# Kernel tuning notes

Measured on AMD Instinct MI355X. Metric: run time of the kernel, lower is better.

## Reference

```python
import jax, jax.numpy as jnp
import numpy as np

N_NODES = 100000
N_EDGES = 1600000
NEG_SLOPE = 0.2


def gat_layer(x, edge_index, W, att_src, att_dst, bias, concat):
    """PyG-style GATConv (v1) with self-loops added, dropout=0."""
    N = x.shape[0]
    H, C = att_src.shape
    ar = jnp.arange(N)
    src = jnp.concatenate([edge_index[0], ar])  # add self-loops
    dst = jnp.concatenate([edge_index[1], ar])
    h = (x @ W).reshape(N, H, C)                # [N,H,C]
    a_src = jnp.sum(h * att_src[None], axis=-1)  # [N,H]
    a_dst = jnp.sum(h * att_dst[None], axis=-1)  # [N,H]
    e = jax.nn.leaky_relu(a_src[src] + a_dst[dst], NEG_SLOPE)  # [E,H]
    # segment softmax over destination nodes
    m = jax.ops.segment_max(e, dst, num_segments=N)
    e = jnp.exp(e - m[dst])
    s = jax.ops.segment_sum(e, dst, num_segments=N)
    alpha = e / (s[dst] + 1e-16)                # [E,H]
    msg = h[src] * alpha[:, :, None]            # [E,H,C]
    out = jax.ops.segment_sum(msg, dst, num_segments=N)  # [N,H,C]
    if concat:
        out = out.reshape(N, H * C)
    else:
        out = out.mean(axis=1)
    return out + bias


def prelu(x, a):
    return jnp.where(x >= 0, x, a * x)


def setup_inputs() -> dict:
    key = jax.random.key(0)
    ks = jax.random.split(key, 12)
    def g(k, shape, fan):
        return jax.random.normal(k, shape, dtype=jnp.float32) * (1.0 / np.sqrt(fan))
    x = jax.random.normal(ks[0], (N_NODES, 256), dtype=jnp.float32)
    edge_index = jax.random.randint(ks[1], (2, N_EDGES), 0, N_NODES, dtype=jnp.int64 if jax.config.read('jax_enable_x64') else jnp.int32)
    return {
        'x': x,
        'edge_index': edge_index,
        'W1': g(ks[2], (256, 64), 256), 'as1': g(ks[3], (8, 8), 8), 'ad1': g(ks[4], (8, 8), 8), 'b1': jnp.zeros((64,), jnp.float32),
        'W2': g(ks[5], (320, 64), 320), 'as2': g(ks[6], (8, 8), 8), 'ad2': g(ks[7], (8, 8), 8), 'b2': jnp.zeros((64,), jnp.float32),
        'W3': g(ks[8], (64, 128), 64), 'as3': g(ks[9], (8, 16), 16), 'ad3': g(ks[10], (8, 16), 16), 'b3': jnp.zeros((16,), jnp.float32),
        'p1': jnp.full((1,), 0.25, jnp.float32), 'p2': jnp.full((1,), 0.25, jnp.float32),
    }


def reference(x, edge_index, W1, as1, ad1, b1, W2, as2, ad2, b2, W3, as3, ad3, b3, p1, p2):
    h = gat_layer(x, edge_index, W1, as1, ad1, b1, concat=True)
    h = prelu(h, p1)
    h = gat_layer(jnp.concatenate([x, h], axis=1), edge_index, W2, as2, ad2, b2, concat=True)
    h = prelu(h, p2)
    h = gat_layer(h, edge_index, W3, as3, ad3, b3, concat=False)
    return jax.nn.log_softmax(h, axis=1)
```

## Files before the change

kernel.cpp:

```cpp
#include <hip/hip_runtime.h>
#include <hip/hip_bf16.h>
#include <stdint.h>

typedef unsigned short u16;
typedef __attribute__((ext_vector_type(8))) short short8;
typedef __attribute__((ext_vector_type(8))) __bf16 bf16x8;
typedef __attribute__((ext_vector_type(4))) float f32x4;
typedef __attribute__((ext_vector_type(4))) float fv4;

#define DEV static __device__ __forceinline__

DEV float bf2f(u16 u) { uint32_t i = ((uint32_t)u) << 16; float f; __builtin_memcpy(&f, &i, 4); return f; }
DEV u16 f2bf(float f) {
    uint32_t i; __builtin_memcpy(&i, &f, 4);
    uint32_t r = i + 0x7FFFu + ((i >> 16) & 1u);
    return (u16)(r >> 16);
}
DEV float lo16f(uint32_t u) { uint32_t i = u << 16; float f; __builtin_memcpy(&f, &i, 4); return f; }
DEV float hi16f(uint32_t u) { uint32_t i = u & 0xFFFF0000u; float f; __builtin_memcpy(&f, &i, 4); return f; }
DEV uint32_t pack2(float a, float b) { return (uint32_t)f2bf(a) | ((uint32_t)f2bf(b) << 16); }
DEV float lrelu(float x) { return x >= 0.f ? x : 0.2f * x; }

#define CHK 4096
#define BN2SH 10
#define BN2 1024

__global__ __launch_bounds__(256) void k_cvt(const float* __restrict__ in, u16* __restrict__ out, int n4) {
    int i = blockIdx.x * 256 + threadIdx.x;
    if (i < n4) {
        fv4 v = __builtin_nontemporal_load((const fv4*)in + i);
        ushort4 o;
        o.x = f2bf(v.x); o.y = f2bf(v.y); o.z = f2bf(v.z); o.w = f2bf(v.w);
        ((ushort4*)out)[i] = o;
    }
}

__global__ __launch_bounds__(256) void k_hist(const int* __restrict__ dst, int* __restrict__ hist,
                                              int NBUK, int nbp, int E) {
    __shared__ int h[BN2];
    int tid = threadIdx.x;
    for (int i = tid; i < NBUK; i += 256) h[i] = 0;
    __syncthreads();
    int b0 = blockIdx.x * CHK;
    int jend = b0 + CHK < E ? b0 + CHK : E;
    for (int j = b0 + tid; j < jend; j += 256)
        atomicAdd(&h[dst[j] >> BN2SH], 1);
    __syncthreads();
    for (int i = tid; i < NBUK; i += 256) hist[i * nbp + blockIdx.x] = h[i];
}

__global__ void k_scanpart(const int* __restrict__ deg, int* __restrict__ bsum, int n) {
    __shared__ int buf[1024];
    int tid = threadIdx.x;
    int i = blockIdx.x * 1024 + tid;
    int v = (i < n) ? deg[i] : 0;
    buf[tid] = v; __syncthreads();
    for (int d = 512; d > 0; d >>= 1) {
        if (tid < d) buf[tid] += buf[tid + d];
        __syncthreads();
    }
    if (tid == 0) bsum[blockIdx.x] = buf[0];
}

__global__ void k_scanbsum(int* bsum, int nb) {
    if (threadIdx.x == 0) {
        int run = 0;
        for (int b = 0; b < nb; ++b) { int t = bsum[b]; bsum[b] = run; run += t; }
    }
}

__global__ void k_scanonly(const int* __restrict__ in, const int* __restrict__ bsum,
                           int* __restrict__ out, int n) {
    __shared__ int buf[1024];
    int tid = threadIdx.x;
    int i = blockIdx.x * 1024 + tid;
    int v = (i < n) ? in[i] : 0;
    buf[tid] = v; __syncthreads();
    for (int d = 1; d < 1024; d <<= 1) {
        int t = (tid >= d) ? buf[tid - d] : 0;
        __syncthreads();
        buf[tid] += t;
        __syncthreads();
    }
    if (i < n) out[i] = buf[tid] - v + bsum[blockIdx.x];
}

__global__ __launch_bounds__(256) void k_part(const int* __restrict__ src, const int* __restrict__ dst,
                                              const int* __restrict__ scanned, int2* __restrict__ stage,
                                              int NBUK, int nbp, int E) {
    __shared__ int cur[BN2];
    int tid = threadIdx.x;
    for (int i = tid; i < NBUK; i += 256) cur[i] = scanned[i * nbp + blockIdx.x];
    __syncthreads();
    int b0 = blockIdx.x * CHK;
    int jend = b0 + CHK < E ? b0 + CHK : E;
    for (int j = b0 + tid; j < jend; j += 256) {
        int d = dst[j];
        int p = atomicAdd(&cur[d >> BN2SH], 1);
        stage[p] = make_int2(src[j], d);
    }
}

__global__ __launch_bounds__(256) void k_csr(const int2* __restrict__ stage, const int* __restrict__ scanned,
                                             int* __restrict__ off, int* __restrict__ srt,
                                             int NBUK, int nbp, int N, int E) {
    __shared__ int deg[BN2];
    __shared__ int ex[BN2];
    __shared__ int tsum[256];
    int tid = threadIdx.x, b = blockIdx.x;
    int base = b << BN2SH;
    int s0 = scanned[b * nbp];
    int s1 = (b + 1 < NBUK) ? scanned[(b + 1) * nbp] : E;
    for (int i = tid; i < BN2; i += 256) deg[i] = 0;
    __syncthreads();
    for (int j = s0 + tid; j < s1; j += 256) atomicAdd(&deg[stage[j].y - base], 1);
    __syncthreads();
    int t4 = tid * 4;
    int d0 = deg[t4], d1 = deg[t4 + 1], d2 = deg[t4 + 2], d3 = deg[t4 + 3];
    int tot = d0 + d1 + d2 + d3;
    tsum[tid] = tot; __syncthreads();
    for (int d = 1; d < 256; d <<= 1) {
        int t = (tid >= d) ? tsum[tid - d] : 0;
        __syncthreads();
        tsum[tid] += t;
        __syncthreads();
    }
    int ebase = tsum[tid] - tot;
    ex[t4] = ebase; ex[t4 + 1] = ebase + d0; ex[t4 + 2] = ebase + d0 + d1; ex[t4 + 3] = ebase + d0 + d1 + d2;
    __syncthreads();
    for (int i = tid; i < BN2; i += 256) { int n = base + i; if (n < N) off[n] = s0 + ex[i]; }
    if (b == 0 && tid == 0) off[N] = E;
    __syncthreads();
    for (int j = s0 + tid; j < s1; j += 256) {
        int2 sd = stage[j];
        int p = atomicAdd(&ex[sd.y - base], 1);
        srt[s0 + p] = sd.x;
    }
}

__global__ __launch_bounds__(256) void gemm_k(const u16* __restrict__ A1, int K1,
                                              const u16* __restrict__ A2, int K2,
                                              const float* __restrict__ W, int M,
                                              u16* __restrict__ out, int N) {
    __shared__ u16 wt[64][328];
    __shared__ u16 As[64][40];
    const int K = K1 + K2;
    const int tid = threadIdx.x;
    const int n0 = blockIdx.x * 64;
    const int cb = blockIdx.y * 64;

    for (int idx = tid; idx < K * 64; idx += 256) {
        int k = idx >> 6, m = idx & 63;
        wt[m][k] = f2bf(W[(size_t)k * M + cb + m]);
    }

    const int wv = tid >> 6, lane = tid & 63;
    const int quad = lane >> 4, r = lane & 15;
    f32x4 acc[4];
#pragma unroll
    for (int ct = 0; ct < 4; ++ct) acc[ct] = (f32x4){0.f, 0.f, 0.f, 0.f};

    const int row = tid >> 2, seg = tid & 3;
    const int gl = n0 + row;

    for (int k0 = 0; k0 < K; k0 += 32) {
        int4 v = {0, 0, 0, 0};
        if (gl < N) {
            const u16* base = (k0 < K1) ? (A1 + (size_t)gl * K1 + k0)
                                        : (A2 + (size_t)gl * K2 + (k0 - K1));
            v = *(const int4*)(base + seg * 8);
        }
        *(int4*)&As[row][seg * 8] = v;
        __syncthreads();
        bf16x8 a = __builtin_bit_cast(bf16x8, *(const short8*)&As[wv * 16 + r][quad * 8]);
#pragma unroll
        for (int ct = 0; ct < 4; ++ct) {
            bf16x8 b = __builtin_bit_cast(bf16x8, *(const short8*)&wt[ct * 16 + r][k0 + quad * 8]);
            acc[ct] = __builtin_amdgcn_mfma_f32_16x16x32_bf16(a, b, acc[ct], 0, 0, 0);
        }
        __syncthreads();
    }

#pragma unroll
    for (int ct = 0; ct < 4; ++ct)
#pragma unroll
        for (int rg = 0; rg < 4; ++rg) {
            int grow = n0 + wv * 16 + quad * 4 + rg;
            if (grow < N) out[(size_t)grow * M + cb + ct * 16 + r] = f2bf(acc[ct][rg]);
        }
}

__global__ __launch_bounds__(256) void acomp8(const u16* __restrict__ g,
                                              const float* __restrict__ ats, const float* __restrict__ atd,
                                              float* __restrict__ a_src, float* __restrict__ a_dst, int N) {
    int lane = threadIdx.x & 63;
    int node = blockIdx.x * 4 + (threadIdx.x >> 6);
    if (node >= N) return;
    float val = bf2f(g[(size_t)node * 64 + lane]);
    float ps = val * ats[lane];
    float pd = val * atd[lane];
#pragma unroll
    for (int d = 1; d < 8; d <<= 1) { ps += __shfl_xor(ps, d); pd += __shfl_xor(pd, d); }
    if ((lane & 7) == 0) {
        a_src[node * 8 + (lane >> 3)] = ps;
        a_dst[node * 8 + (lane >> 3)] = pd;
    }
}

__global__ __launch_bounds__(256) void acomp16(const u16* __restrict__ g,
                                               const float* __restrict__ ats, const float* __restrict__ atd,
                                               float* __restrict__ a_src, float* __restrict__ a_dst, int N) {
    int lane = threadIdx.x & 63;
    int node = blockIdx.x * 4 + (threadIdx.x >> 6);
    if (node >= N) return;
    float v0 = bf2f(g[(size_t)node * 128 + lane]);
    float v1 = bf2f(g[(size_t)node * 128 + lane + 64]);
    float ps0 = v0 * ats[lane],      pd0 = v0 * atd[lane];
    float ps1 = v1 * ats[lane + 64], pd1 = v1 * atd[lane + 64];
#pragma unroll
    for (int d = 1; d < 16; d <<= 1) {
        ps0 += __shfl_xor(ps0, d); pd0 += __shfl_xor(pd0, d);
        ps1 += __shfl_xor(ps1, d); pd1 += __shfl_xor(pd1, d);
    }
    if ((lane & 15) == 0) {
        int hd = lane >> 4;
        a_src[node * 8 + hd] = ps0;     a_dst[node * 8 + hd] = pd0;
        a_src[node * 8 + hd + 4] = ps1; a_dst[node * 8 + hd + 4] = pd1;
    }
}

__global__ __launch_bounds__(256) void agg12(const u16* __restrict__ g,
                                             const float* __restrict__ a_src, const float* __restrict__ a_dst,
                                             const int* __restrict__ off, const int* __restrict__ srt,
                                             const float* __restrict__ bias, const float* __restrict__ pslope,
                                             u16* __restrict__ hout, int N) {
    int tid = threadIdx.x;
    int lane32 = tid & 31;
    int node = blockIdx.x * 8 + (tid >> 5);
    int nd = node < N ? node : N - 1;
    int hd = lane32 >> 2;
    int hw = lane32 & 7;
    int e4 = lane32 >> 3;
    float ad_acc = a_dst[nd * 8 + hd];
    float ad_w   = a_dst[nd * 8 + hw];
    float ws = __expf(lrelu(a_src[nd * 8 + hd] + ad_acc));
    uint32_t gs = *(const uint32_t*)(g + (size_t)nd * 64 + lane32 * 2);
    float s = ws;
    float acc0 = ws * lo16f(gs), acc1 = ws * hi16f(gs);
    int jb = off[nd], je = off[nd + 1];
    int addrH = (tid & 32) * 4;
    int addrW = addrH + hd * 4;
    for (int j = jb; j < je; j += 4) {
        int cnt = je - j;
        int jj = j + e4;
        int idx = srt[jj < je ? jj : (je - 1)];
        float w = __expf(lrelu(a_src[idx * 8 + hw] + ad_w));
        int wi = __builtin_bit_cast(int, w);
#pragma unroll
        for (int t = 0; t < 4; ++t) {
            int srcv = __builtin_amdgcn_ds_bpermute(addrH + t * 32, idx);
            int wvi  = __builtin_amdgcn_ds_bpermute(addrW + t * 32, wi);
            float wv = (t < cnt) ? __builtin_bit_cast(float, wvi) : 0.f;
            uint32_t gv = *(const uint32_t*)(g + (size_t)srcv * 64 + lane32 * 2);
            s += wv;
            acc0 += wv * lo16f(gv);
            acc1 += wv * hi16f(gv);
        }
    }
    float r = 1.f / (s + 1e-16f);
    float2 bv = *(const float2*)(bias + lane32 * 2);
    float p = pslope[0];
    float v0 = acc0 * r + bv.x; v0 = v0 >= 0.f ? v0 : p * v0;
    float v1 = acc1 * r + bv.y; v1 = v1 >= 0.f ? v1 : p * v1;
    if (node < N) *(uint32_t*)(hout + (size_t)node * 64 + lane32 * 2) = pack2(v0, v1);
}

__global__ __launch_bounds__(256) void agg3(const u16* __restrict__ g,
                                            const float* __restrict__ a_src, const float* __restrict__ a_dst,
                                            const int* __restrict__ off, const int* __restrict__ srt,
                                            const float* __restrict__ b3, float* __restrict__ out, int N) {
    int tid = threadIdx.x;
    int lane = tid & 63;
    int node = blockIdx.x * 4 + (tid >> 6);
    int nd = node < N ? node : N - 1;
    int hd = lane >> 3;
    int hw = lane & 7;
    float ad_acc = a_dst[nd * 8 + hd];
    float ad_w   = a_dst[nd * 8 + hw];
    float ws = __expf(lrelu(a_src[nd * 8 + hd] + ad_acc));
    uint32_t gs = *(const uint32_t*)(g + (size_t)nd * 128 + lane * 2);
    float s = ws;
    float acc0 = ws * lo16f(gs), acc1 = ws * hi16f(gs);
    int jb = off[nd], je = off[nd + 1];
    int addrW = hd * 4;
    for (int j = jb; j < je; j += 8) {
        int cnt = je - j;
        int jj = j + hd;
        int idx = srt[jj < je ? jj : (je - 1)];
        float w = __expf(lrelu(a_src[idx * 8 + hw] + ad_w));
        int wi = __builtin_bit_cast(int, w);
#pragma unroll
        for (int t = 0; t < 8; ++t) {
            int srcv = __builtin_amdgcn_readlane(idx, t * 8);
            int wvi  = __builtin_amdgcn_ds_bpermute(addrW + t * 32, wi);
            float wv = (t < cnt) ? __builtin_bit_cast(float, wvi) : 0.f;
            uint32_t gv = *(const uint32_t*)(g + (size_t)srcv * 128 + lane * 2);
            s += wv;
            acc0 += wv * lo16f(gv);
            acc1 += wv * hi16f(gv);
        }
    }
    float r = 1.f / (s + 1e-16f);
    float v0 = acc0 * r, v1 = acc1 * r;
    v0 += __shfl_xor(v0, 8);  v1 += __shfl_xor(v1, 8);
    v0 += __shfl_xor(v0, 16); v1 += __shfl_xor(v1, 16);
    v0 += __shfl_xor(v0, 32); v1 += __shfl_xor(v1, 32);
    int c0 = (lane & 7) * 2;
    float2 bv = *(const float2*)(b3 + c0);
    float mean0 = v0 * 0.125f + bv.x, mean1 = v1 * 0.125f + bv.y;
    float m = fmaxf(mean0, mean1);
    m = fmaxf(m, __shfl_xor(m, 1)); m = fmaxf(m, __shfl_xor(m, 2)); m = fmaxf(m, __shfl_xor(m, 4));
    float se = __expf(mean0 - m) + __expf(mean1 - m);
    se += __shfl_xor(se, 1); se += __shfl_xor(se, 2); se += __shfl_xor(se, 4);
    float lg = __logf(se);
    if (node < N && lane < 8) {
        float2 o; o.x = mean0 - m - lg; o.y = mean1 - m - lg;
        *(float2*)(out + (size_t)node * 16 + c0) = o;
    }
}

extern "C" void kernel_launch(void* const* d_in, const int* in_sizes, int n_in,
                              void* d_out, int out_size, void* d_ws, size_t ws_size,
                              hipStream_t stream) {
    (void)n_in; (void)out_size; (void)ws_size;
    const float* x  = (const float*)d_in[0];
    const int* ei   = (const int*)d_in[1];
    const float* W1 = (const float*)d_in[2];
    const float* as1 = (const float*)d_in[3];
    const float* ad1 = (const float*)d_in[4];
    const float* b1  = (const float*)d_in[5];
    const float* W2  = (const float*)d_in[6];
    const float* as2 = (const float*)d_in[7];
    const float* ad2 = (const float*)d_in[8];
    const float* b2  = (const float*)d_in[9];
    const float* W3  = (const float*)d_in[10];
    const float* as3 = (const float*)d_in[11];
    const float* ad3 = (const float*)d_in[12];
    const float* b3  = (const float*)d_in[13];
    const float* p1  = (const float*)d_in[14];
    const float* p2  = (const float*)d_in[15];
    const int N = in_sizes[0] / 256;
    const int E = in_sizes[1] / 2;
    const int NBUK = (N + BN2 - 1) >> BN2SH;
    const int nbp = (E + CHK - 1) / CHK;
    const int nsc = NBUK * nbp;

    char* ws = (char*)d_ws;
    size_t o = 0;
    auto alloc = [&](size_t bytes) { void* p = ws + o; o = (o + bytes + 255) & ~(size_t)255; return p; };
    int* off     = (int*)alloc((size_t)(N + 1) * 4);
    int* bsum    = (int*)alloc(4096);
    int* hist    = (int*)alloc((size_t)nsc * 4);
    int* scanned = (int*)alloc((size_t)nsc * 4);
    int* srt     = (int*)alloc((size_t)E * 4);
    int2* stage  = (int2*)alloc((size_t)E * 8);
    u16* xb      = (u16*)alloc((size_t)N * 256 * 2);
    u16* g       = (u16*)alloc((size_t)N * 128 * 2);
    float* a_src = (float*)alloc((size_t)N * 8 * 4);
    float* a_dst = (float*)alloc((size_t)N * 8 * 4);
    u16* h1      = (u16*)alloc((size_t)N * 64 * 2);
    u16* h2      = (u16*)alloc((size_t)N * 64 * 2);

    int n4 = N * 256 / 4;
    k_cvt<<<(n4 + 255) / 256, 256, 0, stream>>>(x, xb, n4);

    k_hist<<<nbp, 256, 0, stream>>>(ei + E, hist, NBUK, nbp, E);
    int nS = (nsc + 1023) / 1024;
    k_scanpart<<<nS, 1024, 0, stream>>>(hist, bsum, nsc);
    k_scanbsum<<<1, 64, 0, stream>>>(bsum, nS);
    k_scanonly<<<nS, 1024, 0, stream>>>(hist, bsum, scanned, nsc);
    k_part<<<nbp, 256, 0, stream>>>(ei, ei + E, scanned, stage, NBUK, nbp, E);
    k_csr<<<NBUK, 256, 0, stream>>>(stage, scanned, off, srt, NBUK, nbp, N, E);

    int nb64 = (N + 63) / 64;
    int nb4 = (N + 3) / 4;
    int nb8 = (N + 7) / 8;

    gemm_k<<<dim3(nb64, 1), 256, 0, stream>>>(xb, 256, (const u16*)nullptr, 0, W1, 64, g, N);
    acomp8<<<nb4, 256, 0, stream>>>(g, as1, ad1, a_src, a_dst, N);
    agg12<<<nb8, 256, 0, stream>>>(g, a_src, a_dst, off, srt, b1, p1, h1, N);

    gemm_k<<<dim3(nb64, 1), 256, 0, stream>>>(xb, 256, h1, 64, W2, 64, g, N);
    acomp8<<<nb4, 256, 0, stream>>>(g, as2, ad2, a_src, a_dst, N);
    agg12<<<nb8, 256, 0, stream>>>(g, a_src, a_dst, off, srt, b2, p2, h2, N);

    gemm_k<<<dim3(nb64, 2), 256, 0, stream>>>(h2, 64, (const u16*)nullptr, 0, W3, 128, g, N);
    acomp16<<<nb4, 256, 0, stream>>>(g, as3, ad3, a_src, a_dst, N);
    agg3<<<nb4, 256, 0, stream>>>(g, a_src, a_dst, off, srt, b3, (float*)d_out, N);
}
```

Measured before the change: 572.6 us.

## Restructure GAT aggregation to split edges across lanes with 16-byte gathers

The agg12 and agg3 kernels are rewritten so that each wavefront spreads a node's incoming edges across lane slots. Each lane gathers a full 16-byte chunk of a source row (8 bf16 channels) instead of 4 bytes. The per-slot partial sums are then combined with xor-shuffle reductions, which replaces the bpermute/readlane broadcast of indices and weights. This aims to issue fewer, wider memory requests and keep more edges in flight, at the cost of more registers and a reduction tail. The fp32-to-bf16 conversion kernel also switches to a single packed nontemporal 64-bit store.

```diff
diff --git a/kernel.cpp b/kernel.cpp
--- a/kernel.cpp
+++ b/kernel.cpp
@@ -29,9 +29,9 @@
     int i = blockIdx.x * 256 + threadIdx.x;
     if (i < n4) {
         fv4 v = __builtin_nontemporal_load((const fv4*)in + i);
-        ushort4 o;
-        o.x = f2bf(v.x); o.y = f2bf(v.y); o.z = f2bf(v.z); o.w = f2bf(v.w);
-        ((ushort4*)out)[i] = o;
+        uint64_t o = (uint64_t)f2bf(v.x) | ((uint64_t)f2bf(v.y) << 16)
+                   | ((uint64_t)f2bf(v.z) << 32) | ((uint64_t)f2bf(v.w) << 48);
+        __builtin_nontemporal_store(o, (uint64_t*)out + i);
     }
 }
 
@@ -229,50 +229,86 @@
     }
 }
 
+#define ACC8(gv, wgt) do { float _w = (wgt); \
+    s += _w; \
+    acc0 += _w * lo16f((gv).x); acc1 += _w * hi16f((gv).x); \
+    acc2 += _w * lo16f((gv).y); acc3 += _w * hi16f((gv).y); \
+    acc4 += _w * lo16f((gv).z); acc5 += _w * hi16f((gv).z); \
+    acc6 += _w * lo16f((gv).w); acc7 += _w * hi16f((gv).w); \
+} while (0)
+
+#define RED8(d) do { \
+    s    += __shfl_xor(s,    d); \
+    acc0 += __shfl_xor(acc0, d); acc1 += __shfl_xor(acc1, d); \
+    acc2 += __shfl_xor(acc2, d); acc3 += __shfl_xor(acc3, d); \
+    acc4 += __shfl_xor(acc4, d); acc5 += __shfl_xor(acc5, d); \
+    acc6 += __shfl_xor(acc6, d); acc7 += __shfl_xor(acc7, d); \
+} while (0)
+
+#define REDA(d) do { \
+    acc0 += __shfl_xor(acc0, d); acc1 += __shfl_xor(acc1, d); \
+    acc2 += __shfl_xor(acc2, d); acc3 += __shfl_xor(acc3, d); \
+    acc4 += __shfl_xor(acc4, d); acc5 += __shfl_xor(acc5, d); \
+    acc6 += __shfl_xor(acc6, d); acc7 += __shfl_xor(acc7, d); \
+} while (0)
+
 __global__ __launch_bounds__(256) void agg12(const u16* __restrict__ g,
                                              const float* __restrict__ a_src, const float* __restrict__ a_dst,
                                              const int* __restrict__ off, const int* __restrict__ srt,
                                              const float* __restrict__ bias, const float* __restrict__ pslope,
                                              u16* __restrict__ hout, int N) {
     int tid = threadIdx.x;
-    int lane32 = tid & 31;
-    int node = blockIdx.x * 8 + (tid >> 5);
+    int lane = tid & 63;
+    int node = blockIdx.x * 4 + (tid >> 6);
     int nd = node < N ? node : N - 1;
-    int hd = lane32 >> 2;
-    int hw = lane32 & 7;
-    int e4 = lane32 >> 3;
-    float ad_acc = a_dst[nd * 8 + hd];
-    float ad_w   = a_dst[nd * 8 + hw];
-    float ws = __expf(lrelu(a_src[nd * 8 + hd] + ad_acc));
-    uint32_t gs = *(const uint32_t*)(g + (size_t)nd * 64 + lane32 * 2);
-    float s = ws;
-    float acc0 = ws * lo16f(gs), acc1 = ws * hi16f(gs);
+    int cls = lane & 7;
+    int slot = lane >> 3;
+    float ad = a_dst[nd * 8 + cls];
+    float ws = __expf(lrelu(a_src[nd * 8 + cls] + ad));
+    float m0 = (slot == 0) ? ws : 0.f;
+    uint4 gs = *(const uint4*)((const char*)g + ((size_t)nd << 7) + (cls << 4));
+    float s = m0;
+    float acc0 = m0 * lo16f(gs.x), acc1 = m0 * hi16f(gs.x);
+    float acc2 = m0 * lo16f(gs.y), acc3 = m0 * hi16f(gs.y);
+    float acc4 = m0 * lo16f(gs.z), acc5 = m0 * hi16f(gs.z);
+    float acc6 = m0 * lo16f(gs.w), acc7 = m0 * hi16f(gs.w);
     int jb = off[nd], je = off[nd + 1];
-    int addrH = (tid & 32) * 4;
-    int addrW = addrH + hd * 4;
-    for (int j = jb; j < je; j += 4) {
+    for (int j = jb; j < je; j += 16) {
         int cnt = je - j;
-        int jj = j + e4;
-        int idx = srt[jj < je ? jj : (je - 1)];
-        float w = __expf(lrelu(a_src[idx * 8 + hw] + ad_w));
-        int wi = __builtin_bit_cast(int, w);
-#pragma unroll
-        for (int t = 0; t < 4; ++t) {
-            int srcv = __builtin_amdgcn_ds_bpermute(addrH + t * 32, idx);
-            int wvi  = __builtin_amdgcn_ds_bpermute(addrW + t * 32, wi);
-            float wv = (t < cnt) ? __builtin_bit_cast(float, wvi) : 0.f;
-            uint32_t gv = *(const uint32_t*)(g + (size_t)srcv * 64 + lane32 * 2);
-            s += wv;
-            acc0 += wv * lo16f(gv);
-            acc1 += wv * hi16f(gv);
+        int jj0 = j + slot;
+        int i0 = srt[jj0 < je ? jj0 : je - 1];
+        float w0 = __expf(lrelu(a_src[i0 * 8 + cls] + ad));
+        if (jj0 >= je) w0 = 0.f;
+        uint4 g0 = *(const uint4*)((const char*)g + ((size_t)(uint32_t)i0 << 7) + (cls << 4));
+        if (cnt > 8) {
+            int jj1 = jj0 + 8;
+            int i1 = srt[jj1 < je ? jj1 : je - 1];
+            float w1 = __expf(lrelu(a_src[i1 * 8 + cls] + ad));
+            if (jj1 >= je) w1 = 0.f;
+            uint4 g1 = *(const uint4*)((const char*)g + ((size_t)(uint32_t)i1 << 7) + (cls << 4));
+            ACC8(g0, w0);
+            ACC8(g1, w1);
+        } else {
+            ACC8(g0, w0);
         }
     }
-    float r = 1.f / (s + 1e-16f);
-    float2 bv = *(const float2*)(bias + lane32 * 2);
-    float p = pslope[0];
-    float v0 = acc0 * r + bv.x; v0 = v0 >= 0.f ? v0 : p * v0;
-    float v1 = acc1 * r + bv.y; v1 = v1 >= 0.f ? v1 : p * v1;
-    if (node < N) *(uint32_t*)(hout + (size_t)node * 64 + lane32 * 2) = pack2(v0, v1);
+    RED8(8); RED8(16); RED8(32);
+    if (node < N && slot == 0) {
+        float r = 1.f / (s + 1e-16f);
+        float p = pslope[0];
+        const float* bp = bias + cls * 8;
+        float v0 = acc0 * r + bp[0]; v0 = v0 >= 0.f ? v0 : p * v0;
+        float v1 = acc1 * r + bp[1]; v1 = v1 >= 0.f ? v1 : p * v1;
+        float v2 = acc2 * r + bp[2]; v2 = v2 >= 0.f ? v2 : p * v2;
+        float v3 = acc3 * r + bp[3]; v3 = v3 >= 0.f ? v3 : p * v3;
+        float v4 = acc4 * r + bp[4]; v4 = v4 >= 0.f ? v4 : p * v4;
+        float v5 = acc5 * r + bp[5]; v5 = v5 >= 0.f ? v5 : p * v5;
+        float v6 = acc6 * r + bp[6]; v6 = v6 >= 0.f ? v6 : p * v6;
+        float v7 = acc7 * r + bp[7]; v7 = v7 >= 0.f ? v7 : p * v7;
+        uint4 o;
+        o.x = pack2(v0, v1); o.y = pack2(v2, v3); o.z = pack2(v4, v5); o.w = pack2(v6, v7);
+        *(uint4*)((char*)hout + ((size_t)node << 7) + (cls << 4)) = o;
+    }
 }
 
 __global__ __launch_bounds__(256) void agg3(const u16* __restrict__ g,
@@ -283,49 +319,65 @@
     int lane = tid & 63;
     int node = blockIdx.x * 4 + (tid >> 6);
     int nd = node < N ? node : N - 1;
-    int hd = lane >> 3;
-    int hw = lane & 7;
-    float ad_acc = a_dst[nd * 8 + hd];
-    float ad_w   = a_dst[nd * 8 + hw];
-    float ws = __expf(lrelu(a_src[nd * 8 + hd] + ad_acc));
-    uint32_t gs = *(const uint32_t*)(g + (size_t)nd * 128 + lane * 2);
-    float s = ws;
-    float acc0 = ws * lo16f(gs), acc1 = ws * hi16f(gs);
+    int q = lane & 15;
+    int slot = lane >> 4;
+    int hd = q >> 1;
+    float ad = a_dst[nd * 8 + hd];
+    float ws = __expf(lrelu(a_src[nd * 8 + hd] + ad));
+    float m0 = (slot == 0) ? ws : 0.f;
+    uint4 gs = *(const uint4*)((const char*)g + ((size_t)nd << 8) + (q << 4));
+    float s = m0;
+    float acc0 = m0 * lo16f(gs.x), acc1 = m0 * hi16f(gs.x);
+    float acc2 = m0 * lo16f(gs.y), acc3 = m0 * hi16f(gs.y);
+    float acc4 = m0 * lo16f(gs.z), acc5 = m0 * hi16f(gs.z);
+    float acc6 = m0 * lo16f(gs.w), acc7 = m0 * hi16f(gs.w);
     int jb = off[nd], je = off[nd + 1];
-    int addrW = hd * 4;
     for (int j = jb; j < je; j += 8) {
         int cnt = je - j;
-        int jj = j + hd;
-        int idx = srt[jj < je ? jj : (je - 1)];
-        float w = __expf(lrelu(a_src[idx * 8 + hw] + ad_w));
-        int wi = __builtin_bit_cast(int, w);
-#pragma unroll
-        for (int t = 0; t < 8; ++t) {
-            int srcv = __builtin_amdgcn_readlane(idx, t * 8);
-            int wvi  = __builtin_amdgcn_ds_bpermute(addrW + t * 32, wi);
-            float wv = (t < cnt) ? __builtin_bit_cast(float, wvi) : 0.f;
-            uint32_t gv = *(const uint32_t*)(g + (size_t)srcv * 128 + lane * 2);
-            s += wv;
-            acc0 += wv * lo16f(gv);
-            acc1 += wv * hi16f(gv);
+        int jj0 = j + slot;
+        int i0 = srt[jj0 < je ? jj0 : je - 1];
+        float w0 = __expf(lrelu(a_src[i0 * 8 + hd] + ad));
+        if (jj0 >= je) w0 = 0.f;
+        uint4 g0 = *(const uint4*)((const char*)g + ((size_t)(uint32_t)i0 << 8) + (q << 4));
+        if (cnt > 4) {
+            int jj1 = jj0 + 4;
+            int i1 = srt[jj1 < je ? jj1 : je - 1];
+            float w1 = __expf(lrelu(a_src[i1 * 8 + hd] + ad));
+            if (jj1 >= je) w1 = 0.f;
+            uint4 g1 = *(const uint4*)((const char*)g + ((size_t)(uint32_t)i1 << 8) + (q << 4));
+            ACC8(g0, w0);
+            ACC8(g1, w1);
+        } else {
+            ACC8(g0, w0);
         }
     }
+    RED8(16); RED8(32);
     float r = 1.f / (s + 1e-16f);
-    float v0 = acc0 * r, v1 = acc1 * r;
-    v0 += __shfl_xor(v0, 8);  v1 += __shfl_xor(v1, 8);
-    v0 += __shfl_xor(v0, 16); v1 += __shfl_xor(v1, 16);
-    v0 += __shfl_xor(v0, 32); v1 += __shfl_xor(v1, 32);
-    int c0 = (lane & 7) * 2;
-    float2 bv = *(const float2*)(b3 + c0);
-    float mean0 = v0 * 0.125f + bv.x, mean1 = v1 * 0.125f + bv.y;
-    float m = fmaxf(mean0, mean1);
-    m = fmaxf(m, __shfl_xor(m, 1)); m = fmaxf(m, __shfl_xor(m, 2)); m = fmaxf(m, __shfl_xor(m, 4));
-    float se = __expf(mean0 - m) + __expf(mean1 - m);
-    se += __shfl_xor(se, 1); se += __shfl_xor(se, 2); se += __shfl_xor(se, 4);
+    acc0 *= r; acc1 *= r; acc2 *= r; acc3 *= r;
+    acc4 *= r; acc5 *= r; acc6 *= r; acc7 *= r;
+    REDA(2); REDA(4); REDA(8);
+    int b = lane & 1;
+    const float* bp = b3 + b * 8;
+    float v0 = acc0 * 0.125f + bp[0];
+    float v1 = acc1 * 0.125f + bp[1];
+    float v2 = acc2 * 0.125f + bp[2];
+    float v3 = acc3 * 0.125f + bp[3];
+    float v4 = acc4 * 0.125f + bp[4];
+    float v5 = acc5 * 0.125f + bp[5];
+    float v6 = acc6 * 0.125f + bp[6];
+    float v7 = acc7 * 0.125f + bp[7];
+    float m = fmaxf(fmaxf(fmaxf(v0, v1), fmaxf(v2, v3)), fmaxf(fmaxf(v4, v5), fmaxf(v6, v7)));
+    m = fmaxf(m, __shfl_xor(m, 1));
+    float se = __expf(v0 - m) + __expf(v1 - m) + __expf(v2 - m) + __expf(v3 - m)
+             + __expf(v4 - m) + __expf(v5 - m) + __expf(v6 - m) + __expf(v7 - m);
+    se += __shfl_xor(se, 1);
     float lg = __logf(se);
-    if (node < N && lane < 8) {
-        float2 o; o.x = mean0 - m - lg; o.y = mean1 - m - lg;
-        *(float2*)(out + (size_t)node * 16 + c0) = o;
+    if (node < N && lane < 2) {
+        float4 o0, o1;
+        o0.x = v0 - m - lg; o0.y = v1 - m - lg; o0.z = v2 - m - lg; o0.w = v3 - m - lg;
+        o1.x = v4 - m - lg; o1.y = v5 - m - lg; o1.z = v6 - m - lg; o1.w = v7 - m - lg;
+        float4* op = (float4*)(out + (size_t)node * 16 + b * 8);
+        op[0] = o0; op[1] = o1;
     }
 }
 
@@ -384,15 +436,14 @@
 
     int nb64 = (N + 63) / 64;
     int nb4 = (N + 3) / 4;
-    int nb8 = (N + 7) / 8;
 
     gemm_k<<<dim3(nb64, 1), 256, 0, stream>>>(xb, 256, (const u16*)nullptr, 0, W1, 64, g, N);
     acomp8<<<nb4, 256, 0, stream>>>(g, as1, ad1, a_src, a_dst, N);
-    agg12<<<nb8, 256, 0, stream>>>(g, a_src, a_dst, off, srt, b1, p1, h1, N);
+    agg12<<<nb4, 256, 0, stream>>>(g, a_src, a_dst, off, srt, b1, p1, h1, N);
 
     gemm_k<<<dim3(nb64, 1), 256, 0, stream>>>(xb, 256, h1, 64, W2, 64, g, N);
     acomp8<<<nb4, 256, 0, stream>>>(g, as2, ad2, a_src, a_dst, N);
-    agg12<<<nb8, 256, 0, stream>>>(g, a_src, a_dst, off, srt, b2, p2, h2, N);
+    agg12<<<nb4, 256, 0, stream>>>(g, a_src, a_dst, off, srt, b2, p2, h2, N);
 
     gemm_k<<<dim3(nb64, 2), 256, 0, stream>>>(h2, 64, (const u16*)nullptr, 0, W3, 128, g, N);
     acomp16<<<nb4, 256, 0, stream>>>(g, as3, ad3, a_src, a_dst, N);
```

Result: slower. 593.4 us (+3.6%).

## Pack staged edges into 32-bit words and prefetch next edge chunk in aggregation

Applied to the files above, without the earlier changes.

Edge staging during CSR construction now packs the source index (17 bits) and the local destination offset into one 32-bit word, halving the staging buffer traffic. The aggregation kernels software-pipeline the neighbor index and a_src loads for the next chunk of edges while the current chunk is processed, hiding gather latency. The x-to-bf16 conversion uses a nontemporal 64-bit store. The packing assumes node ids fit in 17 bits (N ≤ 131072), which holds for the given size but breaks for larger graphs.

```diff
diff --git a/kernel.cpp b/kernel.cpp
--- a/kernel.cpp
+++ b/kernel.cpp
@@ -29,9 +29,9 @@
     int i = blockIdx.x * 256 + threadIdx.x;
     if (i < n4) {
         fv4 v = __builtin_nontemporal_load((const fv4*)in + i);
-        ushort4 o;
-        o.x = f2bf(v.x); o.y = f2bf(v.y); o.z = f2bf(v.z); o.w = f2bf(v.w);
-        ((ushort4*)out)[i] = o;
+        uint64_t o = (uint64_t)f2bf(v.x) | ((uint64_t)f2bf(v.y) << 16)
+                   | ((uint64_t)f2bf(v.z) << 32) | ((uint64_t)f2bf(v.w) << 48);
+        __builtin_nontemporal_store(o, (uint64_t*)out + i);
     }
 }
 
@@ -86,7 +86,7 @@
 }
 
 __global__ __launch_bounds__(256) void k_part(const int* __restrict__ src, const int* __restrict__ dst,
-                                              const int* __restrict__ scanned, int2* __restrict__ stage,
+                                              const int* __restrict__ scanned, int* __restrict__ stage,
                                               int NBUK, int nbp, int E) {
     __shared__ int cur[BN2];
     int tid = threadIdx.x;
@@ -97,11 +97,11 @@
     for (int j = b0 + tid; j < jend; j += 256) {
         int d = dst[j];
         int p = atomicAdd(&cur[d >> BN2SH], 1);
-        stage[p] = make_int2(src[j], d);
-    }
-}
-
-__global__ __launch_bounds__(256) void k_csr(const int2* __restrict__ stage, const int* __restrict__ scanned,
+        stage[p] = src[j] | ((d & (BN2 - 1)) << 17);
+    }
+}
+
+__global__ __launch_bounds__(256) void k_csr(const int* __restrict__ stage, const int* __restrict__ scanned,
                                              int* __restrict__ off, int* __restrict__ srt,
                                              int NBUK, int nbp, int N, int E) {
     __shared__ int deg[BN2];
@@ -113,7 +113,7 @@
     int s1 = (b + 1 < NBUK) ? scanned[(b + 1) * nbp] : E;
     for (int i = tid; i < BN2; i += 256) deg[i] = 0;
     __syncthreads();
-    for (int j = s0 + tid; j < s1; j += 256) atomicAdd(&deg[stage[j].y - base], 1);
+    for (int j = s0 + tid; j < s1; j += 256) atomicAdd(&deg[(uint32_t)stage[j] >> 17], 1);
     __syncthreads();
     int t4 = tid * 4;
     int d0 = deg[t4], d1 = deg[t4 + 1], d2 = deg[t4 + 2], d3 = deg[t4 + 3];
@@ -132,9 +132,9 @@
     if (b == 0 && tid == 0) off[N] = E;
     __syncthreads();
     for (int j = s0 + tid; j < s1; j += 256) {
-        int2 sd = stage[j];
-        int p = atomicAdd(&ex[sd.y - base], 1);
-        srt[s0 + p] = sd.x;
+        int sd = stage[j];
+        int p = atomicAdd(&ex[(uint32_t)sd >> 17], 1);
+        srt[s0 + p] = sd & 0x1FFFF;
     }
 }
 
@@ -250,12 +250,19 @@
     int jb = off[nd], je = off[nd + 1];
     int addrH = (tid & 32) * 4;
     int addrW = addrH + hd * 4;
+    int idx = 0; float asv = 0.f;
+    if (jb < je) {
+        int jc = jb + e4; jc = jc < je ? jc : je - 1;
+        idx = srt[jc];
+        asv = a_src[idx * 8 + hw];
+    }
     for (int j = jb; j < je; j += 4) {
         int cnt = je - j;
-        int jj = j + e4;
-        int idx = srt[jj < je ? jj : (je - 1)];
-        float w = __expf(lrelu(a_src[idx * 8 + hw] + ad_w));
+        float w = __expf(lrelu(asv + ad_w));
         int wi = __builtin_bit_cast(int, w);
+        int jn = j + 4 + e4; jn = jn < je ? jn : je - 1;
+        int idx_n = srt[jn];
+        float as_n = a_src[idx_n * 8 + hw];
 #pragma unroll
         for (int t = 0; t < 4; ++t) {
             int srcv = __builtin_amdgcn_ds_bpermute(addrH + t * 32, idx);
@@ -266,6 +273,7 @@
             acc0 += wv * lo16f(gv);
             acc1 += wv * hi16f(gv);
         }
+        idx = idx_n; asv = as_n;
     }
     float r = 1.f / (s + 1e-16f);
     float2 bv = *(const float2*)(bias + lane32 * 2);
@@ -293,12 +301,19 @@
     float acc0 = ws * lo16f(gs), acc1 = ws * hi16f(gs);
     int jb = off[nd], je = off[nd + 1];
     int addrW = hd * 4;
+    int idx = 0; float asv = 0.f;
+    if (jb < je) {
+        int jc = jb + hd; jc = jc < je ? jc : je - 1;
+        idx = srt[jc];
+        asv = a_src[idx * 8 + hw];
+    }
     for (int j = jb; j < je; j += 8) {
         int cnt = je - j;
-        int jj = j + hd;
-        int idx = srt[jj < je ? jj : (je - 1)];
-        float w = __expf(lrelu(a_src[idx * 8 + hw] + ad_w));
+        float w = __expf(lrelu(asv + ad_w));
         int wi = __builtin_bit_cast(int, w);
+        int jn = j + 8 + hd; jn = jn < je ? jn : je - 1;
+        int idx_n = srt[jn];
+        float as_n = a_src[idx_n * 8 + hw];
 #pragma unroll
         for (int t = 0; t < 8; ++t) {
             int srcv = __builtin_amdgcn_readlane(idx, t * 8);
@@ -309,6 +324,7 @@
             acc0 += wv * lo16f(gv);
             acc1 += wv * hi16f(gv);
         }
+        idx = idx_n; asv = as_n;
     }
     float r = 1.f / (s + 1e-16f);
     float v0 = acc0 * r, v1 = acc1 * r;
@@ -363,7 +379,7 @@
     int* hist    = (int*)alloc((size_t)nsc * 4);
     int* scanned = (int*)alloc((size_t)nsc * 4);
     int* srt     = (int*)alloc((size_t)E * 4);
-    int2* stage  = (int2*)alloc((size_t)E * 8);
+    int* stage   = (int*)alloc((size_t)E * 4);
     u16* xb      = (u16*)alloc((size_t)N * 256 * 2);
     u16* g       = (u16*)alloc((size_t)N * 128 * 2);
     float* a_src = (float*)alloc((size_t)N * 8 * 4);
```

Result: no change. 577.5 us (+0.9%).
